# Kernel optimization log

Measured on AMD Instinct MI355X. Metric: run time of the kernel, lower is better.

The kernel has to match this reference:

```python
import jax, jax.numpy as jnp
import numpy as np

B, T, D_MODEL, HEAD_DIM = 4, 4096, 1024, 2


def setup_inputs() -> dict:
    key = jax.random.key(0)
    kx, kq, kk, kv = jax.random.split(key, 4)
    x = jax.random.normal(kx, (B, T, D_MODEL), dtype=jnp.float32)
    # nn.Linear weights: (out_features, in_features), applied as x @ W.T
    s_qk = 1.0 / np.sqrt(D_MODEL)
    W_Q = jax.random.uniform(kq, (HEAD_DIM, D_MODEL), minval=-s_qk, maxval=s_qk, dtype=jnp.float32)
    W_K = jax.random.uniform(kk, (HEAD_DIM, D_MODEL), minval=-s_qk, maxval=s_qk, dtype=jnp.float32)
    W_V = jax.random.uniform(kv, (D_MODEL, D_MODEL), minval=-s_qk, maxval=s_qk, dtype=jnp.float32)
    # strict upper-triangular True = masked (future positions)
    causal_mask = jnp.triu(jnp.ones((T, T), dtype=bool), k=1)[None, :, :]
    return {"x": x, "W_Q": W_Q, "W_K": W_K, "W_V": W_V, "causal_mask": causal_mask}


def reference(x, W_Q, W_K, W_V, causal_mask):
    # x: (B, T, d_model)
    Q = jnp.einsum('btd,hd->bth', x, W_Q)   # (B, T, head_dim)
    K = jnp.einsum('bsd,hd->bsh', x, W_K)   # (B, S, head_dim)
    V = jnp.einsum('bsd,ed->bse', x, W_V)   # (B, S, d_model)
    scores = jnp.einsum('bth,bsh->bts', Q, K)              # (B, T, S)
    scores = jnp.where(causal_mask, -jnp.inf, scores)
    max_idx = jnp.argmax(scores, axis=-1)                  # (B, T)
    # one-hot scatter + bmm in the original == hard gather of V rows
    out = jnp.take_along_axis(V, max_idx[..., None], axis=1)  # (B, T, d_model)
    return out
```

## Files before the change

### kernel.cpp

```cpp
#include <hip/hip_runtime.h>
#include <math.h>

#define TT 4096
#define DM 1024
#define BB 4
#define BT (BB * TT)
#define SENTINEL 0x7fffffff


__device__ __forceinline__ float dot4(const float4 a, const float4 b) {
    return a.x * b.x + a.y * b.y + a.z * b.z + a.w * b.w;
}

__global__ __launch_bounds__(256) void qk_kernel(const float* __restrict__ x,
                                                 const float* __restrict__ wq,
                                                 const float* __restrict__ wk,
                                                 float* __restrict__ Q,
                                                 float* __restrict__ K,
                                                 int* __restrict__ rep,
                                                 int* __restrict__ cnt) {
    __shared__ float4 wqs0[256], wqs1[256], wks0[256], wks1[256];
    const int tid = threadIdx.x;
    const int row0 = blockIdx.x * 4;

    wqs0[tid] = ((const float4*)(wq))[tid];
    wqs1[tid] = ((const float4*)(wq + DM))[tid];
    wks0[tid] = ((const float4*)(wk))[tid];
    wks1[tid] = ((const float4*)(wk + DM))[tid];

    if (tid < 4) rep[row0 + tid] = SENTINEL;
    if (blockIdx.x == 0 && tid == 4) cnt[0] = 0;
    __syncthreads();

    const int wave = tid >> 6, lane = tid & 63;
    const int row = row0 + wave;
    const float4* xr = (const float4*)(x + (size_t)row * DM);

    float s0 = 0.f, s1 = 0.f, s2 = 0.f, s3 = 0.f;
    #pragma unroll
    for (int j = 0; j < 4; ++j) {
        const float4 xv = xr[j * 64 + lane];
        s0 += dot4(xv, wqs0[j * 64 + lane]);
        s1 += dot4(xv, wqs1[j * 64 + lane]);
        s2 += dot4(xv, wks0[j * 64 + lane]);
        s3 += dot4(xv, wks1[j * 64 + lane]);
    }
    #pragma unroll
    for (int off = 32; off > 0; off >>= 1) {
        s0 += __shfl_down(s0, off);
        s1 += __shfl_down(s1, off);
        s2 += __shfl_down(s2, off);
        s3 += __shfl_down(s3, off);
    }
    if (lane == 0) {
        ((float2*)Q)[row] = make_float2(s0, s1);
        ((float2*)K)[row] = make_float2(s2, s3);
    }
}

__global__ __launch_bounds__(256) void argmax_kernel(const float* __restrict__ Q,
                                                     const float* __restrict__ K,
                                                     int* __restrict__ idx,
                                                     int* __restrict__ rep,
                                                     int* __restrict__ list,
                                                     int* __restrict__ cnt) {
    __shared__ float2 ks[TT];
    const int b  = blockIdx.x >> 10;
    const int tg = blockIdx.x & 1023;
    const int tid = threadIdx.x;
    const int nfill = tg * 4 + 4;

    const float2* kb = (const float2*)(K + (size_t)b * TT * 2);
    for (int i = tid; i < nfill; i += 256) ks[i] = kb[i];
    __syncthreads();

    const int wave = tid >> 6, lane = tid & 63;
    const int t = tg * 4 + wave;
    const float2 q = ((const float2*)Q)[b * TT + t];
    const float4* kp = (const float4*)ks;

    float best = -INFINITY;
    int bi = 0x7fffffff;
    int p = lane;
    while (2 * (p + 64) + 1 <= t) {
        const float4 a = kp[p];
        const float4 c = kp[p + 64];
        const float c0 = q.x * a.x + q.y * a.y;
        const float c1 = q.x * a.z + q.y * a.w;
        const float c2 = q.x * c.x + q.y * c.y;
        const float c3 = q.x * c.z + q.y * c.w;
        if (c0 > best) { best = c0; bi = 2 * p; }
        if (c1 > best) { best = c1; bi = 2 * p + 1; }
        if (c2 > best) { best = c2; bi = 2 * (p + 64); }
        if (c3 > best) { best = c3; bi = 2 * (p + 64) + 1; }
        p += 128;
    }
    while (2 * p <= t) {
        const float4 a = kp[p];
        const float c0 = q.x * a.x + q.y * a.y;
        if (c0 > best) { best = c0; bi = 2 * p; }
        if (2 * p + 1 <= t) {
            const float c1 = q.x * a.z + q.y * a.w;
            if (c1 > best) { best = c1; bi = 2 * p + 1; }
        }
        p += 64;
    }
    #pragma unroll
    for (int off = 32; off > 0; off >>= 1) {
        const float ov = __shfl_down(best, off);
        const int   oi = __shfl_down(bi, off);
        if (ov > best || (ov == best && oi < bi)) { best = ov; bi = oi; }
    }
    if (lane == 0) {
        idx[b * TT + t] = bi;
        const int old = atomicMin(&rep[b * TT + bi], t);
        if (old == SENTINEL) {
            const int pp = atomicAdd(cnt, 1);
            list[pp] = b * TT + bi;
        }
    }
}

__global__ __launch_bounds__(256) void vrow_kernel(const float* __restrict__ x,
                                                   const float* __restrict__ wv,
                                                   const int* __restrict__ rep,
                                                   const int* __restrict__ list,
                                                   const int* __restrict__ cnt,
                                                   float* __restrict__ out) {
    const int tid = threadIdx.x, wave = tid >> 6, lane = tid & 63;
    const int slice = blockIdx.x >> 4;
    const int usub  = blockIdx.x & 15;
    const int e0 = slice * 16 + wave * 4;

    float4 w[4][4];
    #pragma unroll
    for (int r = 0; r < 4; ++r) {
        const float4* wr = (const float4*)(wv + (size_t)(e0 + r) * DM);
        #pragma unroll
        for (int j = 0; j < 4; ++j) w[r][j] = wr[j * 64 + lane];
    }

    const int n = cnt[0];
    for (int li = usub; li < n; li += 16) {
        const int bs = list[li];
        const int b  = bs >> 12;
        const int r  = rep[bs];
        const float4* xr = (const float4*)(x + (size_t)bs * DM);
        float4 xv[4];
        #pragma unroll
        for (int j = 0; j < 4; ++j) xv[j] = xr[j * 64 + lane];

        float s0 = 0.f, s1 = 0.f, s2 = 0.f, s3 = 0.f;
        #pragma unroll
        for (int j = 0; j < 4; ++j) {
            s0 += dot4(w[0][j], xv[j]);
            s1 += dot4(w[1][j], xv[j]);
            s2 += dot4(w[2][j], xv[j]);
            s3 += dot4(w[3][j], xv[j]);
        }
        #pragma unroll
        for (int off = 32; off > 0; off >>= 1) {
            s0 += __shfl_down(s0, off);
            s1 += __shfl_down(s1, off);
            s2 += __shfl_down(s2, off);
            s3 += __shfl_down(s3, off);
        }
        if (lane == 0)
            *(float4*)(out + ((size_t)(b * TT + r)) * DM + e0) = make_float4(s0, s1, s2, s3);
    }
}

__global__ __launch_bounds__(256) void gather_kernel(const int* __restrict__ idx,
                                                     const int* __restrict__ rep,
                                                     float* __restrict__ out) {
    const int bt = blockIdx.x;
    const int b = bt >> 12, t = bt & (TT - 1);
    const int s = idx[bt];
    const int r = rep[b * TT + s];
    if (r == t) return;
    const float4* src = (const float4*)(out + ((size_t)(b * TT + r)) * DM);
    float4* dst = (float4*)(out + (size_t)bt * DM);
    dst[threadIdx.x] = src[threadIdx.x];
}

extern "C" void kernel_launch(void* const* d_in, const int* in_sizes, int n_in,
                              void* d_out, int out_size, void* d_ws, size_t ws_size,
                              hipStream_t stream) {
    const float* x  = (const float*)d_in[0];
    const float* wq = (const float*)d_in[1];
    const float* wk = (const float*)d_in[2];
    const float* wv = (const float*)d_in[3];
    float* out = (float*)d_out;

    char* ws = (char*)d_ws;
    float* Q    = (float*)(ws);
    float* K    = (float*)(ws + 131072);
    int*   idx  = (int*)  (ws + 262144);
    int*   rep  = (int*)  (ws + 327680);
    int*   list = (int*)  (ws + 393216);
    int*   cnt  = (int*)  (ws + 458752);

    qk_kernel<<<BT / 4, 256, 0, stream>>>(x, wq, wk, Q, K, rep, cnt);
    argmax_kernel<<<4096, 256, 0, stream>>>(Q, K, idx, rep, list, cnt);
    vrow_kernel<<<1024, 256, 0, stream>>>(x, wv, rep, list, cnt, out);
    gather_kernel<<<BT, 256, 0, stream>>>(idx, rep, out);
}
```

Before: 215.5 us.

## Fuse four kernels into one persistent kernel with software grid barriers

Replaces the four launches (QK projection, causal argmax, V-row computation, gather) with a single persistent kernel of 256 blocks that syncs phases through an atomic grid barrier. The argmax phase now interleaves query rows per block for load balance and loads the full K for each batch into LDS once per block. The aim is to remove launch overhead and the small-grid tails of each stage. In exchange it uses far fewer blocks (256 versus thousands), which may reduce latency hiding in the memory-bound projection and gather phases, and it depends on all blocks being co-resident for the barrier.

```diff
diff --git a/kernel.cpp b/kernel.cpp
--- a/kernel.cpp
+++ b/kernel.cpp
@@ -6,181 +6,209 @@
 #define BB 4
 #define BT (BB * TT)
 #define SENTINEL 0x7fffffff
+#define NBLK 256
+#define NTHR 256
 
 
 __device__ __forceinline__ float dot4(const float4 a, const float4 b) {
     return a.x * b.x + a.y * b.y + a.z * b.z + a.w * b.w;
 }
 
-__global__ __launch_bounds__(256) void qk_kernel(const float* __restrict__ x,
-                                                 const float* __restrict__ wq,
-                                                 const float* __restrict__ wk,
-                                                 float* __restrict__ Q,
-                                                 float* __restrict__ K,
-                                                 int* __restrict__ rep,
-                                                 int* __restrict__ cnt) {
-    __shared__ float4 wqs0[256], wqs1[256], wks0[256], wks1[256];
-    const int tid = threadIdx.x;
-    const int row0 = blockIdx.x * 4;
-
-    wqs0[tid] = ((const float4*)(wq))[tid];
-    wqs1[tid] = ((const float4*)(wq + DM))[tid];
-    wks0[tid] = ((const float4*)(wk))[tid];
-    wks1[tid] = ((const float4*)(wk + DM))[tid];
-
-    if (tid < 4) rep[row0 + tid] = SENTINEL;
-    if (blockIdx.x == 0 && tid == 4) cnt[0] = 0;
+__device__ __forceinline__ void grid_barrier(int* bar) {
     __syncthreads();
-
-    const int wave = tid >> 6, lane = tid & 63;
-    const int row = row0 + wave;
-    const float4* xr = (const float4*)(x + (size_t)row * DM);
-
-    float s0 = 0.f, s1 = 0.f, s2 = 0.f, s3 = 0.f;
-    #pragma unroll
-    for (int j = 0; j < 4; ++j) {
-        const float4 xv = xr[j * 64 + lane];
-        s0 += dot4(xv, wqs0[j * 64 + lane]);
-        s1 += dot4(xv, wqs1[j * 64 + lane]);
-        s2 += dot4(xv, wks0[j * 64 + lane]);
-        s3 += dot4(xv, wks1[j * 64 + lane]);
-    }
-    #pragma unroll
-    for (int off = 32; off > 0; off >>= 1) {
-        s0 += __shfl_down(s0, off);
-        s1 += __shfl_down(s1, off);
-        s2 += __shfl_down(s2, off);
-        s3 += __shfl_down(s3, off);
-    }
-    if (lane == 0) {
-        ((float2*)Q)[row] = make_float2(s0, s1);
-        ((float2*)K)[row] = make_float2(s2, s3);
-    }
-}
-
-__global__ __launch_bounds__(256) void argmax_kernel(const float* __restrict__ Q,
-                                                     const float* __restrict__ K,
+    if (threadIdx.x == 0) {
+        __threadfence();
+        const int gen = __hip_atomic_load(&bar[1], __ATOMIC_RELAXED, __HIP_MEMORY_SCOPE_AGENT);
+        if (atomicAdd(&bar[0], 1) == NBLK - 1) {
+            __hip_atomic_store(&bar[0], 0, __ATOMIC_RELAXED, __HIP_MEMORY_SCOPE_AGENT);
+            __threadfence();
+            atomicAdd(&bar[1], 1);
+        } else {
+            while (__hip_atomic_load(&bar[1], __ATOMIC_ACQUIRE, __HIP_MEMORY_SCOPE_AGENT) == gen)
+                __builtin_amdgcn_s_sleep(2);
+        }
+        __threadfence();
+    }
+    __syncthreads();
+}
+
+__global__ __launch_bounds__(NTHR) void fused_kernel(const float* __restrict__ x,
+                                                     const float* __restrict__ wq,
+                                                     const float* __restrict__ wk,
+                                                     const float* __restrict__ wv,
+                                                     float* __restrict__ Q,
+                                                     float* __restrict__ K,
                                                      int* __restrict__ idx,
                                                      int* __restrict__ rep,
                                                      int* __restrict__ list,
-                                                     int* __restrict__ cnt) {
-    __shared__ float2 ks[TT];
-    const int b  = blockIdx.x >> 10;
-    const int tg = blockIdx.x & 1023;
+                                                     int* __restrict__ cnt,
+                                                     int* __restrict__ bar,
+                                                     float* __restrict__ out) {
+    __shared__ float4 ks4[TT / 2];
+    __shared__ int srow[64];
+
     const int tid = threadIdx.x;
-    const int nfill = tg * 4 + 4;
-
-    const float2* kb = (const float2*)(K + (size_t)b * TT * 2);
-    for (int i = tid; i < nfill; i += 256) ks[i] = kb[i];
-    __syncthreads();
-
     const int wave = tid >> 6, lane = tid & 63;
-    const int t = tg * 4 + wave;
-    const float2 q = ((const float2*)Q)[b * TT + t];
-    const float4* kp = (const float4*)ks;
-
-    float best = -INFINITY;
-    int bi = 0x7fffffff;
-    int p = lane;
-    while (2 * (p + 64) + 1 <= t) {
-        const float4 a = kp[p];
-        const float4 c = kp[p + 64];
-        const float c0 = q.x * a.x + q.y * a.y;
-        const float c1 = q.x * a.z + q.y * a.w;
-        const float c2 = q.x * c.x + q.y * c.y;
-        const float c3 = q.x * c.z + q.y * c.w;
-        if (c0 > best) { best = c0; bi = 2 * p; }
-        if (c1 > best) { best = c1; bi = 2 * p + 1; }
-        if (c2 > best) { best = c2; bi = 2 * (p + 64); }
-        if (c3 > best) { best = c3; bi = 2 * (p + 64) + 1; }
-        p += 128;
-    }
-    while (2 * p <= t) {
-        const float4 a = kp[p];
-        const float c0 = q.x * a.x + q.y * a.y;
-        if (c0 > best) { best = c0; bi = 2 * p; }
-        if (2 * p + 1 <= t) {
-            const float c1 = q.x * a.z + q.y * a.w;
-            if (c1 > best) { best = c1; bi = 2 * p + 1; }
-        }
-        p += 64;
-    }
-    #pragma unroll
-    for (int off = 32; off > 0; off >>= 1) {
-        const float ov = __shfl_down(best, off);
-        const int   oi = __shfl_down(bi, off);
-        if (ov > best || (ov == best && oi < bi)) { best = ov; bi = oi; }
-    }
-    if (lane == 0) {
-        idx[b * TT + t] = bi;
-        const int old = atomicMin(&rep[b * TT + bi], t);
-        if (old == SENTINEL) {
-            const int pp = atomicAdd(cnt, 1);
-            list[pp] = b * TT + bi;
-        }
-    }
-}
-
-__global__ __launch_bounds__(256) void vrow_kernel(const float* __restrict__ x,
-                                                   const float* __restrict__ wv,
-                                                   const int* __restrict__ rep,
-                                                   const int* __restrict__ list,
-                                                   const int* __restrict__ cnt,
-                                                   float* __restrict__ out) {
-    const int tid = threadIdx.x, wave = tid >> 6, lane = tid & 63;
-    const int slice = blockIdx.x >> 4;
-    const int usub  = blockIdx.x & 15;
-    const int e0 = slice * 16 + wave * 4;
-
-    float4 w[4][4];
-    #pragma unroll
-    for (int r = 0; r < 4; ++r) {
-        const float4* wr = (const float4*)(wv + (size_t)(e0 + r) * DM);
-        #pragma unroll
-        for (int j = 0; j < 4; ++j) w[r][j] = wr[j * 64 + lane];
-    }
-
-    const int n = cnt[0];
-    for (int li = usub; li < n; li += 16) {
-        const int bs = list[li];
-        const int b  = bs >> 12;
-        const int r  = rep[bs];
-        const float4* xr = (const float4*)(x + (size_t)bs * DM);
-        float4 xv[4];
-        #pragma unroll
-        for (int j = 0; j < 4; ++j) xv[j] = xr[j * 64 + lane];
-
-        float s0 = 0.f, s1 = 0.f, s2 = 0.f, s3 = 0.f;
+    const int bid = blockIdx.x;
+
+    {
+        const int g = bid * NTHR + tid;
+        if (g < BT) rep[g] = SENTINEL;
+        if (g == 0) cnt[0] = 0;
+
+        float4 wq0[4], wq1[4], wk0[4], wk1[4];
         #pragma unroll
         for (int j = 0; j < 4; ++j) {
-            s0 += dot4(w[0][j], xv[j]);
-            s1 += dot4(w[1][j], xv[j]);
-            s2 += dot4(w[2][j], xv[j]);
-            s3 += dot4(w[3][j], xv[j]);
-        }
+            wq0[j] = ((const float4*)(wq))[j * 64 + lane];
+            wq1[j] = ((const float4*)(wq + DM))[j * 64 + lane];
+            wk0[j] = ((const float4*)(wk))[j * 64 + lane];
+            wk1[j] = ((const float4*)(wk + DM))[j * 64 + lane];
+        }
+        const int row0 = bid * 64;
+        for (int i = 0; i < 16; ++i) {
+            const int row = row0 + i * 4 + wave;
+            const float4* xr = (const float4*)(x + (size_t)row * DM);
+            float s0 = 0.f, s1 = 0.f, s2 = 0.f, s3 = 0.f;
+            #pragma unroll
+            for (int j = 0; j < 4; ++j) {
+                const float4 xv = xr[j * 64 + lane];
+                s0 += dot4(xv, wq0[j]);
+                s1 += dot4(xv, wq1[j]);
+                s2 += dot4(xv, wk0[j]);
+                s3 += dot4(xv, wk1[j]);
+            }
+            #pragma unroll
+            for (int off = 32; off > 0; off >>= 1) {
+                s0 += __shfl_down(s0, off);
+                s1 += __shfl_down(s1, off);
+                s2 += __shfl_down(s2, off);
+                s3 += __shfl_down(s3, off);
+            }
+            if (lane == 0) {
+                ((float2*)Q)[row] = make_float2(s0, s1);
+                ((float2*)K)[row] = make_float2(s2, s3);
+            }
+        }
+    }
+    grid_barrier(bar);
+
+    {
+        const int b  = bid >> 6;
+        const int cc = bid & 63;
+        const float4* kb4 = (const float4*)(K + (size_t)b * TT * 2);
+        for (int i = tid; i < TT / 2; i += NTHR) ks4[i] = kb4[i];
+        __syncthreads();
+
+        for (int m = wave; m < 64; m += 4) {
+            const int t = cc + (m << 6);
+            const float2 q = ((const float2*)Q)[b * TT + t];
+
+            float best = -INFINITY;
+            int bi = 0x7fffffff;
+            int p = lane;
+            while (2 * (p + 64) + 1 <= t) {
+                const float4 a = ks4[p];
+                const float4 d = ks4[p + 64];
+                const float c0 = q.x * a.x + q.y * a.y;
+                const float c1 = q.x * a.z + q.y * a.w;
+                const float c2 = q.x * d.x + q.y * d.y;
+                const float c3 = q.x * d.z + q.y * d.w;
+                if (c0 > best) { best = c0; bi = 2 * p; }
+                if (c1 > best) { best = c1; bi = 2 * p + 1; }
+                if (c2 > best) { best = c2; bi = 2 * (p + 64); }
+                if (c3 > best) { best = c3; bi = 2 * (p + 64) + 1; }
+                p += 128;
+            }
+            while (2 * p <= t) {
+                const float4 a = ks4[p];
+                const float c0 = q.x * a.x + q.y * a.y;
+                if (c0 > best) { best = c0; bi = 2 * p; }
+                if (2 * p + 1 <= t) {
+                    const float c1 = q.x * a.z + q.y * a.w;
+                    if (c1 > best) { best = c1; bi = 2 * p + 1; }
+                }
+                p += 64;
+            }
+            #pragma unroll
+            for (int off = 32; off > 0; off >>= 1) {
+                const float ov = __shfl_down(best, off);
+                const int   oi = __shfl_down(bi, off);
+                if (ov > best || (ov == best && oi < bi)) { best = ov; bi = oi; }
+            }
+            if (lane == 0) {
+                idx[b * TT + t] = bi;
+                const int old = atomicMin(&rep[b * TT + bi], t);
+                if (old == SENTINEL) {
+                    const int pp = atomicAdd(cnt, 1);
+                    list[pp] = b * TT + bi;
+                }
+            }
+        }
+    }
+    grid_barrier(bar);
+
+    {
+        const int slice = bid >> 2;
+        const int usub  = bid & 3;
+        const int e0 = slice * 16 + wave * 4;
+
+        float4 w[4][4];
         #pragma unroll
-        for (int off = 32; off > 0; off >>= 1) {
-            s0 += __shfl_down(s0, off);
-            s1 += __shfl_down(s1, off);
-            s2 += __shfl_down(s2, off);
-            s3 += __shfl_down(s3, off);
-        }
-        if (lane == 0)
-            *(float4*)(out + ((size_t)(b * TT + r)) * DM + e0) = make_float4(s0, s1, s2, s3);
-    }
-}
-
-__global__ __launch_bounds__(256) void gather_kernel(const int* __restrict__ idx,
-                                                     const int* __restrict__ rep,
-                                                     float* __restrict__ out) {
-    const int bt = blockIdx.x;
-    const int b = bt >> 12, t = bt & (TT - 1);
-    const int s = idx[bt];
-    const int r = rep[b * TT + s];
-    if (r == t) return;
-    const float4* src = (const float4*)(out + ((size_t)(b * TT + r)) * DM);
-    float4* dst = (float4*)(out + (size_t)bt * DM);
-    dst[threadIdx.x] = src[threadIdx.x];
+        for (int r = 0; r < 4; ++r) {
+            const float4* wr = (const float4*)(wv + (size_t)(e0 + r) * DM);
+            #pragma unroll
+            for (int j = 0; j < 4; ++j) w[r][j] = wr[j * 64 + lane];
+        }
+
+        const int n = cnt[0];
+        for (int li = usub; li < n; li += 4) {
+            const int bs = list[li];
+            const int b  = bs >> 12;
+            const int r  = rep[bs];
+            const float4* xr = (const float4*)(x + (size_t)bs * DM);
+            float4 xv[4];
+            #pragma unroll
+            for (int j = 0; j < 4; ++j) xv[j] = xr[j * 64 + lane];
+
+            float s0 = 0.f, s1 = 0.f, s2 = 0.f, s3 = 0.f;
+            #pragma unroll
+            for (int j = 0; j < 4; ++j) {
+                s0 += dot4(w[0][j], xv[j]);
+                s1 += dot4(w[1][j], xv[j]);
+                s2 += dot4(w[2][j], xv[j]);
+                s3 += dot4(w[3][j], xv[j]);
+            }
+            #pragma unroll
+            for (int off = 32; off > 0; off >>= 1) {
+                s0 += __shfl_down(s0, off);
+                s1 += __shfl_down(s1, off);
+                s2 += __shfl_down(s2, off);
+                s3 += __shfl_down(s3, off);
+            }
+            if (lane == 0)
+                *(float4*)(out + ((size_t)(b * TT + r)) * DM + e0) = make_float4(s0, s1, s2, s3);
+        }
+    }
+    grid_barrier(bar);
+
+    {
+        const int row0 = bid * 64;
+        if (tid < 64) {
+            const int bt = row0 + tid;
+            const int b = bt >> 12;
+            srow[tid] = b * TT + rep[b * TT + idx[bt]];
+        }
+        __syncthreads();
+        #pragma unroll 4
+        for (int i = 0; i < 64; ++i) {
+            const int bt = row0 + i;
+            const int sr = srow[i];
+            if (sr == bt) continue;
+            const float4* src = (const float4*)(out + (size_t)sr * DM);
+            float4* dst = (float4*)(out + (size_t)bt * DM);
+            dst[tid] = src[tid];
+        }
+    }
 }
 
 extern "C" void kernel_launch(void* const* d_in, const int* in_sizes, int n_in,
@@ -199,9 +227,8 @@
     int*   rep  = (int*)  (ws + 327680);
     int*   list = (int*)  (ws + 393216);
     int*   cnt  = (int*)  (ws + 458752);
-
-    qk_kernel<<<BT / 4, 256, 0, stream>>>(x, wq, wk, Q, K, rep, cnt);
-    argmax_kernel<<<4096, 256, 0, stream>>>(Q, K, idx, rep, list, cnt);
-    vrow_kernel<<<1024, 256, 0, stream>>>(x, wv, rep, list, cnt, out);
-    gather_kernel<<<BT, 256, 0, stream>>>(idx, rep, out);
-}
+    int*   bar  = (int*)  (ws + 458760);
+
+    hipMemsetAsync(bar, 0, 8, stream);
+    fused_kernel<<<NBLK, NTHR, 0, stream>>>(x, wq, wk, wv, Q, K, idx, rep, list, cnt, bar, out);
+}
```

Measured after the change: 335.8 us. 55.8% more time.

## Stage unique V rows in compact buffer and gather all output rows in batches

Applied to the files above, without the earlier changes.

Computed V rows now go to a compact workspace buffer indexed by list position, with a vpos map recorded in the argmax kernel. The gather kernel then copies every output row from that buffer, 16 rows per block, instead of one row per block. The QK kernel keeps its weights in registers rather than shared memory and handles 8 rows per block, and the argmax block order is permuted to spread causal work across blocks. In exchange, all output rows are now written by the gather, including ones previously written in place, and an extra workspace buffer is used.

```diff
diff --git a/kernel.cpp b/kernel.cpp
--- a/kernel.cpp
+++ b/kernel.cpp
@@ -19,42 +19,45 @@
                                                  float* __restrict__ K,
                                                  int* __restrict__ rep,
                                                  int* __restrict__ cnt) {
-    __shared__ float4 wqs0[256], wqs1[256], wks0[256], wks1[256];
     const int tid = threadIdx.x;
-    const int row0 = blockIdx.x * 4;
-
-    wqs0[tid] = ((const float4*)(wq))[tid];
-    wqs1[tid] = ((const float4*)(wq + DM))[tid];
-    wks0[tid] = ((const float4*)(wk))[tid];
-    wks1[tid] = ((const float4*)(wk + DM))[tid];
-
-    if (tid < 4) rep[row0 + tid] = SENTINEL;
-    if (blockIdx.x == 0 && tid == 4) cnt[0] = 0;
-    __syncthreads();
-
     const int wave = tid >> 6, lane = tid & 63;
-    const int row = row0 + wave;
-    const float4* xr = (const float4*)(x + (size_t)row * DM);
-
-    float s0 = 0.f, s1 = 0.f, s2 = 0.f, s3 = 0.f;
+    const int row0 = blockIdx.x * 8;
+
+    if (tid < 8) rep[row0 + tid] = SENTINEL;
+    if (row0 == 0 && tid == 8) cnt[0] = 0;
+
+    float4 wq0[4], wq1[4], wk0[4], wk1[4];
     #pragma unroll
     for (int j = 0; j < 4; ++j) {
-        const float4 xv = xr[j * 64 + lane];
-        s0 += dot4(xv, wqs0[j * 64 + lane]);
-        s1 += dot4(xv, wqs1[j * 64 + lane]);
-        s2 += dot4(xv, wks0[j * 64 + lane]);
-        s3 += dot4(xv, wks1[j * 64 + lane]);
-    }
-    #pragma unroll
-    for (int off = 32; off > 0; off >>= 1) {
-        s0 += __shfl_down(s0, off);
-        s1 += __shfl_down(s1, off);
-        s2 += __shfl_down(s2, off);
-        s3 += __shfl_down(s3, off);
-    }
-    if (lane == 0) {
-        ((float2*)Q)[row] = make_float2(s0, s1);
-        ((float2*)K)[row] = make_float2(s2, s3);
+        wq0[j] = ((const float4*)(wq))[j * 64 + lane];
+        wq1[j] = ((const float4*)(wq + DM))[j * 64 + lane];
+        wk0[j] = ((const float4*)(wk))[j * 64 + lane];
+        wk1[j] = ((const float4*)(wk + DM))[j * 64 + lane];
+    }
+    #pragma unroll
+    for (int i = 0; i < 2; ++i) {
+        const int row = row0 + i * 4 + wave;
+        const float4* xr = (const float4*)(x + (size_t)row * DM);
+        float s0 = 0.f, s1 = 0.f, s2 = 0.f, s3 = 0.f;
+        #pragma unroll
+        for (int j = 0; j < 4; ++j) {
+            const float4 xv = xr[j * 64 + lane];
+            s0 += dot4(xv, wq0[j]);
+            s1 += dot4(xv, wq1[j]);
+            s2 += dot4(xv, wk0[j]);
+            s3 += dot4(xv, wk1[j]);
+        }
+        #pragma unroll
+        for (int off = 32; off > 0; off >>= 1) {
+            s0 += __shfl_down(s0, off);
+            s1 += __shfl_down(s1, off);
+            s2 += __shfl_down(s2, off);
+            s3 += __shfl_down(s3, off);
+        }
+        if (lane == 0) {
+            ((float2*)Q)[row] = make_float2(s0, s1);
+            ((float2*)K)[row] = make_float2(s2, s3);
+        }
     }
 }
 
@@ -63,10 +66,12 @@
                                                      int* __restrict__ idx,
                                                      int* __restrict__ rep,
                                                      int* __restrict__ list,
+                                                     int* __restrict__ vpos,
                                                      int* __restrict__ cnt) {
     __shared__ float2 ks[TT];
-    const int b  = blockIdx.x >> 10;
-    const int tg = blockIdx.x & 1023;
+    const int b   = blockIdx.x >> 10;
+    const int tgr = blockIdx.x & 1023;
+    const int tg  = ((tgr & 31) << 5) | (tgr >> 5);
     const int tid = threadIdx.x;
     const int nfill = tg * 4 + 4;
 
@@ -113,20 +118,21 @@
     }
     if (lane == 0) {
         idx[b * TT + t] = bi;
-        const int old = atomicMin(&rep[b * TT + bi], t);
+        const int bs = b * TT + bi;
+        const int old = atomicMin(&rep[bs], t);
         if (old == SENTINEL) {
             const int pp = atomicAdd(cnt, 1);
-            list[pp] = b * TT + bi;
+            list[pp] = bs;
+            vpos[bs] = pp;
         }
     }
 }
 
 __global__ __launch_bounds__(256) void vrow_kernel(const float* __restrict__ x,
                                                    const float* __restrict__ wv,
-                                                   const int* __restrict__ rep,
                                                    const int* __restrict__ list,
                                                    const int* __restrict__ cnt,
-                                                   float* __restrict__ out) {
+                                                   float* __restrict__ vrows) {
     const int tid = threadIdx.x, wave = tid >> 6, lane = tid & 63;
     const int slice = blockIdx.x >> 4;
     const int usub  = blockIdx.x & 15;
@@ -143,8 +149,6 @@
     const int n = cnt[0];
     for (int li = usub; li < n; li += 16) {
         const int bs = list[li];
-        const int b  = bs >> 12;
-        const int r  = rep[bs];
         const float4* xr = (const float4*)(x + (size_t)bs * DM);
         float4 xv[4];
         #pragma unroll
@@ -166,21 +170,29 @@
             s3 += __shfl_down(s3, off);
         }
         if (lane == 0)
-            *(float4*)(out + ((size_t)(b * TT + r)) * DM + e0) = make_float4(s0, s1, s2, s3);
+            *(float4*)(vrows + (size_t)li * DM + e0) = make_float4(s0, s1, s2, s3);
     }
 }
 
 __global__ __launch_bounds__(256) void gather_kernel(const int* __restrict__ idx,
-                                                     const int* __restrict__ rep,
+                                                     const int* __restrict__ vpos,
+                                                     const float* __restrict__ vrows,
                                                      float* __restrict__ out) {
-    const int bt = blockIdx.x;
-    const int b = bt >> 12, t = bt & (TT - 1);
-    const int s = idx[bt];
-    const int r = rep[b * TT + s];
-    if (r == t) return;
-    const float4* src = (const float4*)(out + ((size_t)(b * TT + r)) * DM);
-    float4* dst = (float4*)(out + (size_t)bt * DM);
-    dst[threadIdx.x] = src[threadIdx.x];
+    __shared__ int sli[16];
+    const int tid = threadIdx.x;
+    const int row0 = blockIdx.x * 16;
+    if (tid < 16) {
+        const int bt = row0 + tid;
+        const int b = bt >> 12;
+        sli[tid] = vpos[b * TT + idx[bt]];
+    }
+    __syncthreads();
+    #pragma unroll 4
+    for (int i = 0; i < 16; ++i) {
+        const float4* src = (const float4*)(vrows + (size_t)sli[i] * DM);
+        float4* dst = (float4*)(out + (size_t)(row0 + i) * DM);
+        dst[tid] = src[tid];
+    }
 }
 
 extern "C" void kernel_launch(void* const* d_in, const int* in_sizes, int n_in,
@@ -193,15 +205,17 @@
     float* out = (float*)d_out;
 
     char* ws = (char*)d_ws;
-    float* Q    = (float*)(ws);
-    float* K    = (float*)(ws + 131072);
-    int*   idx  = (int*)  (ws + 262144);
-    int*   rep  = (int*)  (ws + 327680);
-    int*   list = (int*)  (ws + 393216);
-    int*   cnt  = (int*)  (ws + 458752);
-
-    qk_kernel<<<BT / 4, 256, 0, stream>>>(x, wq, wk, Q, K, rep, cnt);
-    argmax_kernel<<<4096, 256, 0, stream>>>(Q, K, idx, rep, list, cnt);
-    vrow_kernel<<<1024, 256, 0, stream>>>(x, wv, rep, list, cnt, out);
-    gather_kernel<<<BT, 256, 0, stream>>>(idx, rep, out);
-}
+    float* Q     = (float*)(ws);
+    float* K     = (float*)(ws + 131072);
+    int*   idx   = (int*)  (ws + 262144);
+    int*   rep   = (int*)  (ws + 327680);
+    int*   list  = (int*)  (ws + 393216);
+    int*   vpos  = (int*)  (ws + 458752);
+    int*   cnt   = (int*)  (ws + 524288);
+    float* vrows = (float*)(ws + 1048576);
+
+    qk_kernel<<<BT / 8, 256, 0, stream>>>(x, wq, wk, Q, K, rep, cnt);
+    argmax_kernel<<<4096, 256, 0, stream>>>(Q, K, idx, rep, list, vpos, cnt);
+    vrow_kernel<<<1024, 256, 0, stream>>>(x, wv, list, cnt, vrows);
+    gather_kernel<<<BT / 16, 256, 0, stream>>>(idx, vpos, vrows, out);
+}
```

New measurement: 222.2 us. +3.1%, slower.
